# Kernel optimization log

Hardware: AMD Instinct MI355X
Metric: run time of the kernel (lower is better)

Reference implementation:

```python
import jax, jax.numpy as jnp
import numpy as np

N_CELL = 50000
N_GENE = 50000
E = 800000
D = 256
EPS = 1e-5


def setup_inputs() -> dict:
    key = jax.random.key(0)
    ks = jax.random.split(key, 12)
    inp = {
        "x_cell": jax.random.normal(ks[0], (N_CELL, D), jnp.float32),
        "x_gene": jax.random.normal(ks[1], (N_GENE, D), jnp.float32),
        "W_cg": jax.random.normal(ks[2], (D, D), jnp.float32) * (1.0 / np.sqrt(D)),
        "W_gc": jax.random.normal(ks[3], (D, D), jnp.float32) * (1.0 / np.sqrt(D)),
        "W_gg": jax.random.normal(ks[4], (D, D), jnp.float32) * (1.0 / np.sqrt(D)),
        "gamma_cell": jnp.ones((D,), jnp.float32),
        "beta_cell": jnp.zeros((D,), jnp.float32),
        "gamma_gene": jnp.ones((D,), jnp.float32),
        "beta_gene": jnp.zeros((D,), jnp.float32),
        "b_cell": jnp.zeros((D,), jnp.float32),
        "b_gene": jnp.zeros((D,), jnp.float32),
        "src_cg": jax.random.randint(ks[5], (E,), 0, N_CELL, jnp.int64 if jax.config.jax_enable_x64 else jnp.int32),
        "dst_cg": jax.random.randint(ks[6], (E,), 0, N_GENE, jnp.int64 if jax.config.jax_enable_x64 else jnp.int32),
        "src_gc": jax.random.randint(ks[7], (E,), 0, N_GENE, jnp.int64 if jax.config.jax_enable_x64 else jnp.int32),
        "dst_gc": jax.random.randint(ks[8], (E,), 0, N_CELL, jnp.int64 if jax.config.jax_enable_x64 else jnp.int32),
        "src_gg": jax.random.randint(ks[9], (E,), 0, N_GENE, jnp.int64 if jax.config.jax_enable_x64 else jnp.int32),
        "dst_gg": jax.random.randint(ks[10], (E,), 0, N_GENE, jnp.int64 if jax.config.jax_enable_x64 else jnp.int32),
    }
    return inp


def _graph_conv(x_src, src, dst, n_src, n_dst, W):
    """DGL GraphConv with norm='both': D_dst^{-1/2} A D_src^{-1/2} X W."""
    ones = jnp.ones(src.shape[0], x_src.dtype)
    deg_out = jnp.clip(jax.ops.segment_sum(ones, src, num_segments=n_src), 1.0)
    deg_in = jnp.clip(jax.ops.segment_sum(ones, dst, num_segments=n_dst), 1.0)
    h = x_src * jax.lax.rsqrt(deg_out)[:, None]          # [n_src, D]
    agg = jax.ops.segment_sum(h[src], dst, num_segments=n_dst)  # gather+scatter
    agg = agg * jax.lax.rsqrt(deg_in)[:, None]           # [n_dst, D]
    return agg @ W


def _post(h, gamma, beta, b):
    # LayerNorm (affine) -> + h_bias -> relu -> dropout(p=0, eval = identity)
    mu = jnp.mean(h, axis=-1, keepdims=True)
    var = jnp.mean((h - mu) ** 2, axis=-1, keepdims=True)
    h = (h - mu) * jax.lax.rsqrt(var + EPS) * gamma + beta
    return jax.nn.relu(h + b)


def reference(x_cell, x_gene, W_cg, W_gc, W_gg, gamma_cell, beta_cell,
              gamma_gene, beta_gene, b_cell, b_gene,
              src_cg, dst_cg, src_gc, dst_gc, src_gg, dst_gg):
    # HeteroGraphConv with aggregate='sum' across relations per dst ntype
    h_gene = (_graph_conv(x_cell, src_cg, dst_cg, N_CELL, N_GENE, W_cg)
              + _graph_conv(x_gene, src_gg, dst_gg, N_GENE, N_GENE, W_gg))
    h_cell = _graph_conv(x_gene, src_gc, dst_gc, N_GENE, N_CELL, W_gc)
    out_cell = _post(h_cell, gamma_cell, beta_cell, b_cell)
    out_gene = _post(h_gene, gamma_gene, beta_gene, b_gene)
    return jnp.stack([out_cell, out_gene])  # [2, 50000, 256]
```

## Files before the change

### kernel.cpp

```cpp
#include <hip/hip_runtime.h>
#include <hip/hip_bf16.h>
#include <stdint.h>

#define DDIM 256
#define NSHARD 8
#define T1 4096
#define NCPAD 128
#define CCAP 9216

typedef short s8v __attribute__((ext_vector_type(8)));
typedef float f4v __attribute__((ext_vector_type(4)));

__device__ __forceinline__ float bf2f(unsigned u) { return __uint_as_float(u << 16); }
__device__ __forceinline__ unsigned short f2bf(float f) {
    __hip_bfloat16 h = __float2bfloat16(f);
    return *reinterpret_cast<unsigned short*>(&h);
}
__device__ __forceinline__ unsigned pack2(float a, float b) {
    return (unsigned)f2bf(a) | ((unsigned)f2bf(b) << 16);
}

__global__ void transpose3_k(const float* __restrict__ W0, const float* __restrict__ W1,
                             const float* __restrict__ W2, __hip_bfloat16* __restrict__ T0,
                             __hip_bfloat16* __restrict__ T1v, __hip_bfloat16* __restrict__ T2) {
    const float* W = (blockIdx.y == 0) ? W0 : (blockIdx.y == 1) ? W1 : W2;
    __hip_bfloat16* T = (blockIdx.y == 0) ? T0 : (blockIdx.y == 1) ? T1v : T2;
    T[blockIdx.x * DDIM + threadIdx.x] = __float2bfloat16(W[threadIdx.x * DDIM + blockIdx.x]);
}

__global__ __launch_bounds__(256) void bin1_k(
    const int* __restrict__ s0, const int* __restrict__ d0,
    const int* __restrict__ s1, const int* __restrict__ d1,
    const int* __restrict__ s2, const int* __restrict__ d2,
    int* __restrict__ cs_shard,
    int* __restrict__ gcur,
    unsigned* __restrict__ recs,
    int N, int E) {
    __shared__ unsigned stage[T1];
    __shared__ int hcnt[NCPAD], hoff[NCPAD], lbase[NCPAD], lcur[NCPAD];
    const int t = threadIdx.x;
    const int rel = blockIdx.y;
    const int* s = (rel == 0) ? s0 : (rel == 1) ? s1 : s2;
    const int* d = (rel == 0) ? d0 : (rel == 1) ? d1 : d2;
    const int e0 = blockIdx.x * T1;
    const int n = min(T1, E - e0);
    int* csb = cs_shard + ((size_t)(blockIdx.x & (NSHARD - 1)) * 3 + rel) * N;

    if (t < NCPAD) { hcnt[t] = 0; lcur[t] = 0; }
    __syncthreads();

    int ssr[T1 / 256], ddr[T1 / 256];
    #pragma unroll
    for (int k = 0; k < T1 / 256; ++k) {
        const int li = k * 256 + t;
        const bool v = li < n;
        ssr[k] = v ? s[e0 + li] : -1;
        ddr[k] = v ? d[e0 + li] : -1;
        if (v) {
            atomicAdd(&hcnt[ddr[k] >> 9], 1);
            atomicAdd(&csb[ssr[k]], 1);
        }
    }
    __syncthreads();

    if (t < 64) {
        const int a0 = hcnt[2 * t], a1 = hcnt[2 * t + 1];
        const int sum = a0 + a1;
        int incl = sum;
        #pragma unroll
        for (int off = 1; off < 64; off <<= 1) {
            const int u = __shfl_up(incl, off);
            if (t >= off) incl += u;
        }
        const int excl = incl - sum;
        hoff[2 * t] = excl;
        hoff[2 * t + 1] = excl + a0;
    }
    __syncthreads();
    if (t < NCPAD) lbase[t] = atomicAdd(&gcur[rel * NCPAD + t], hcnt[t]);
    __syncthreads();

    #pragma unroll
    for (int k = 0; k < T1 / 256; ++k) {
        if (ddr[k] >= 0) {
            const int b = ddr[k] >> 9;
            const int p = atomicAdd(&lcur[b], 1);
            stage[hoff[b] + p] = (unsigned)ssr[k] | ((unsigned)(ddr[k] & 511) << 16)
                                 | ((unsigned)b << 25);
        }
    }
    __syncthreads();

    for (int i = t; i < n; i += 256) {
        const unsigned r = stage[i];
        const int b = (int)(r >> 25);
        const int pos = lbase[b] + (i - hoff[b]);
        if (pos < CCAP)
            recs[((size_t)rel * NCPAD + b) * CCAP + pos] = r & 0x1FFFFFFu;
    }
}

__device__ __forceinline__ int deg_sum(const int* __restrict__ cs_shard, int rel, int r, int N) {
    int v = 0;
    #pragma unroll
    for (int s = 0; s < NSHARD; ++s) v += cs_shard[((size_t)s * 3 + rel) * N + r];
    return v;
}


__device__ void sort_body(int sb, unsigned char* smem,
                          const unsigned* __restrict__ recs32,
                          unsigned short* __restrict__ recs16,
                          const int* __restrict__ gcur,
                          int* __restrict__ row_beg, int* __restrict__ row_cnt,
                          int N, int ncb) {
    unsigned short* stage = (unsigned short*)smem;
    int* rc   = (int*)(smem + 18432);
    int* ro   = (int*)(smem + 20480);
    int* rcur = (int*)(smem + 22528);
    const int t = threadIdx.x;
    const int rel = sb / ncb, bin = sb % ncb;
    const size_t base = ((size_t)rel * NCPAD + bin) * CCAP;
    const int n = min(gcur[rel * NCPAD + bin], CCAP);

    for (int i = t; i < 512; i += 256) rc[i] = 0;
    __syncthreads();
    for (int i = t; i < n; i += 256)
        atomicAdd(&rc[(recs32[base + i] >> 16) & 511], 1);
    __syncthreads();
    if (t < 64) {
        int v[8], p[8], sum = 0;
        #pragma unroll
        for (int j = 0; j < 8; ++j) { v[j] = rc[t * 8 + j]; p[j] = sum; sum += v[j]; }
        int incl = sum;
        #pragma unroll
        for (int off = 1; off < 64; off <<= 1) {
            const int u = __shfl_up(incl, off);
            if (t >= off) incl += u;
        }
        const int excl = incl - sum;
        #pragma unroll
        for (int j = 0; j < 8; ++j) { ro[t * 8 + j] = excl + p[j]; rcur[t * 8 + j] = excl + p[j]; }
    }
    __syncthreads();
    for (int i = t; i < 512; i += 256) {
        const int grow = bin * 512 + i;
        if (grow < N) {
            row_cnt[(size_t)rel * N + grow] = rc[i];
            row_beg[(size_t)rel * N + grow] = (int)(base + ro[i]);
        }
    }
    for (int i = t; i < n; i += 256) {
        const unsigned r = recs32[base + i];
        const int pos = atomicAdd(&rcur[(r >> 16) & 511], 1);
        stage[pos] = (unsigned short)(r & 0xffffu);
    }
    __syncthreads();
    for (int i = t; i < n; i += 256)
        recs16[base + i] = stage[i];
}

__device__ void gemm2_body(int gb, unsigned char* smem, const float* __restrict__ X,
                           const __hip_bfloat16* __restrict__ Wt0,
                           const __hip_bfloat16* __restrict__ Wt1,
                           const int* __restrict__ cs_shard, int rel0, int rel1,
                           __hip_bfloat16* __restrict__ Y0, __hip_bfloat16* __restrict__ Y1,
                           int M, int N) {
    typedef __hip_bfloat16 (*lds_t)[2][16][DDIM];
    lds_t wlds = (lds_t)smem;
    const int t = threadIdx.x;
    const int lane = t & 63, wid = t >> 6;
    const int c = lane & 15, kb = lane >> 4;
    const int rA = gb * 128 + wid * 32 + c;
    const int rB = rA + 16;
    const bool vA = rA < M, vB = rB < M;
    const int rAc = vA ? rA : (M - 1), rBc = vB ? rB : (M - 1);

    s8v xfA[8], xfB[8];
    const float* xA = X + (size_t)rAc * DDIM;
    const float* xB = X + (size_t)rBc * DDIM;
    #pragma unroll
    for (int ks = 0; ks < 8; ++ks) {
        const int k0 = ks * 32 + kb * 8;
        const f4v a0 = *reinterpret_cast<const f4v*>(xA + k0);
        const f4v a1 = *reinterpret_cast<const f4v*>(xA + k0 + 4);
        const f4v b0 = *reinterpret_cast<const f4v*>(xB + k0);
        const f4v b1 = *reinterpret_cast<const f4v*>(xB + k0 + 4);
        union { s8v v; unsigned short u[8]; } fa, fb;
        #pragma unroll
        for (int j = 0; j < 4; ++j) {
            fa.u[j] = f2bf(a0[j]); fa.u[4 + j] = f2bf(a1[j]);
            fb.u[j] = f2bf(b0[j]); fb.u[4 + j] = f2bf(b1[j]);
        }
        xfA[ks] = fa.v; xfB[ks] = fb.v;
    }

    const int dA0 = deg_sum(cs_shard, rel0, rAc, N), dB0 = deg_sum(cs_shard, rel0, rBc, N);
    const int dA1 = deg_sum(cs_shard, rel1, rAc, N), dB1 = deg_sum(cs_shard, rel1, rBc, N);
    const float s0A = rsqrtf((float)(dA0 < 1 ? 1 : dA0));
    const float s0B = rsqrtf((float)(dB0 < 1 ? 1 : dB0));
    const float s1A = rsqrtf((float)(dA1 < 1 ? 1 : dA1));
    const float s1B = rsqrtf((float)(dB1 < 1 ? 1 : dB1));

    {
        #pragma unroll
        for (int j = 0; j < 4; ++j) {
            const int q = t + j * 256;
            const int rel = q >> 9, rt = (q >> 5) & 15, ch = q & 31;
            const __hip_bfloat16* Wsrc = rel ? Wt1 : Wt0;
            const uint4 v = *reinterpret_cast<const uint4*>(Wsrc + (size_t)rt * DDIM + ch * 8);
            *reinterpret_cast<uint4*>(&(*wlds)[0 * 2 + rel][rt][(ch ^ (rt & 7)) * 8]) = v;
        }
    }

    #pragma unroll 2
    for (int nt = 0; nt < 16; ++nt) {
        __syncthreads();
        uint4 sv[4];
        if (nt + 1 < 16) {
            #pragma unroll
            for (int j = 0; j < 4; ++j) {
                const int q = t + j * 256;
                const int rel = q >> 9, rt = (q >> 5) & 15, ch = q & 31;
                const __hip_bfloat16* Wsrc = rel ? Wt1 : Wt0;
                sv[j] = *reinterpret_cast<const uint4*>(
                    Wsrc + (size_t)((nt + 1) * 16 + rt) * DDIM + ch * 8);
            }
        }

        const int buf = nt & 1;
        f4v a00 = (f4v){0.f,0.f,0.f,0.f}, a01 = a00, a10 = a00, a11 = a00;
        #pragma unroll
        for (int ks = 0; ks < 8; ++ks) {
            const int chs = ((kb + 4 * ks) ^ (c & 7)) * 8;
            const s8v wf0 = *reinterpret_cast<const s8v*>(&(*wlds)[buf * 2 + 0][c][chs]);
            const s8v wf1 = *reinterpret_cast<const s8v*>(&(*wlds)[buf * 2 + 1][c][chs]);
            a00 = __builtin_amdgcn_mfma_f32_16x16x32_bf16(wf0, xfA[ks], a00, 0, 0, 0);
            a10 = __builtin_amdgcn_mfma_f32_16x16x32_bf16(wf0, xfB[ks], a10, 0, 0, 0);
            a01 = __builtin_amdgcn_mfma_f32_16x16x32_bf16(wf1, xfA[ks], a01, 0, 0, 0);
            a11 = __builtin_amdgcn_mfma_f32_16x16x32_bf16(wf1, xfB[ks], a11, 0, 0, 0);
        }
        const int col = nt * 16 + kb * 4;
        if (vA) {
            uint2 o0, o1;
            o0.x = pack2(a00[0] * s0A, a00[1] * s0A); o0.y = pack2(a00[2] * s0A, a00[3] * s0A);
            o1.x = pack2(a01[0] * s1A, a01[1] * s1A); o1.y = pack2(a01[2] * s1A, a01[3] * s1A);
            *reinterpret_cast<uint2*>(Y0 + (size_t)rA * DDIM + col) = o0;
            *reinterpret_cast<uint2*>(Y1 + (size_t)rA * DDIM + col) = o1;
        }
        if (vB) {
            uint2 o0, o1;
            o0.x = pack2(a10[0] * s0B, a10[1] * s0B); o0.y = pack2(a10[2] * s0B, a10[3] * s0B);
            o1.x = pack2(a11[0] * s1B, a11[1] * s1B); o1.y = pack2(a11[2] * s1B, a11[3] * s1B);
            *reinterpret_cast<uint2*>(Y0 + (size_t)rB * DDIM + col) = o0;
            *reinterpret_cast<uint2*>(Y1 + (size_t)rB * DDIM + col) = o1;
        }

        if (nt + 1 < 16) {
            #pragma unroll
            for (int j = 0; j < 4; ++j) {
                const int q = t + j * 256;
                const int rel = q >> 9, rt = (q >> 5) & 15, ch = q & 31;
                *reinterpret_cast<uint4*>(&(*wlds)[(buf ^ 1) * 2 + rel][rt][(ch ^ (rt & 7)) * 8]) = sv[j];
            }
        }
    }
}

__device__ void gemm1_body(int gb, unsigned char* smem, const float* __restrict__ X,
                           const __hip_bfloat16* __restrict__ Wt0,
                           const int* __restrict__ cs_shard, int rel0,
                           __hip_bfloat16* __restrict__ Y0, int M, int N) {
    typedef __hip_bfloat16 (*lds_t)[16][DDIM];
    lds_t wlds = (lds_t)smem;
    const int t = threadIdx.x;
    const int lane = t & 63, wid = t >> 6;
    const int c = lane & 15, kb = lane >> 4;
    const int rA = gb * 128 + wid * 32 + c;
    const int rB = rA + 16;
    const bool vA = rA < M, vB = rB < M;
    const int rAc = vA ? rA : (M - 1), rBc = vB ? rB : (M - 1);

    s8v xfA[8], xfB[8];
    const float* xA = X + (size_t)rAc * DDIM;
    const float* xB = X + (size_t)rBc * DDIM;
    #pragma unroll
    for (int ks = 0; ks < 8; ++ks) {
        const int k0 = ks * 32 + kb * 8;
        const f4v a0 = *reinterpret_cast<const f4v*>(xA + k0);
        const f4v a1 = *reinterpret_cast<const f4v*>(xA + k0 + 4);
        const f4v b0 = *reinterpret_cast<const f4v*>(xB + k0);
        const f4v b1 = *reinterpret_cast<const f4v*>(xB + k0 + 4);
        union { s8v v; unsigned short u[8]; } fa, fb;
        #pragma unroll
        for (int j = 0; j < 4; ++j) {
            fa.u[j] = f2bf(a0[j]); fa.u[4 + j] = f2bf(a1[j]);
            fb.u[j] = f2bf(b0[j]); fb.u[4 + j] = f2bf(b1[j]);
        }
        xfA[ks] = fa.v; xfB[ks] = fb.v;
    }
    const int dA0 = deg_sum(cs_shard, rel0, rAc, N), dB0 = deg_sum(cs_shard, rel0, rBc, N);
    const float s0A = rsqrtf((float)(dA0 < 1 ? 1 : dA0));
    const float s0B = rsqrtf((float)(dB0 < 1 ? 1 : dB0));

    {
        #pragma unroll
        for (int j = 0; j < 2; ++j) {
            const int q = t + j * 256;
            const int rt = (q >> 5) & 15, ch = q & 31;
            const uint4 v = *reinterpret_cast<const uint4*>(Wt0 + (size_t)rt * DDIM + ch * 8);
            *reinterpret_cast<uint4*>(&(*wlds)[0 * 16 + rt][(ch ^ (rt & 7)) * 8]) = v;
        }
    }

    #pragma unroll 2
    for (int nt = 0; nt < 16; ++nt) {
        __syncthreads();
        uint4 sv[2];
        if (nt + 1 < 16) {
            #pragma unroll
            for (int j = 0; j < 2; ++j) {
                const int q = t + j * 256;
                const int rt = (q >> 5) & 15, ch = q & 31;
                sv[j] = *reinterpret_cast<const uint4*>(
                    Wt0 + (size_t)((nt + 1) * 16 + rt) * DDIM + ch * 8);
            }
        }

        const int buf = nt & 1;
        f4v a00 = (f4v){0.f,0.f,0.f,0.f}, a10 = a00;
        #pragma unroll
        for (int ks = 0; ks < 8; ++ks) {
            const int chs = ((kb + 4 * ks) ^ (c & 7)) * 8;
            const s8v wf0 = *reinterpret_cast<const s8v*>(&(*wlds)[buf * 16 + c][chs]);
            a00 = __builtin_amdgcn_mfma_f32_16x16x32_bf16(wf0, xfA[ks], a00, 0, 0, 0);
            a10 = __builtin_amdgcn_mfma_f32_16x16x32_bf16(wf0, xfB[ks], a10, 0, 0, 0);
        }
        const int col = nt * 16 + kb * 4;
        if (vA) {
            uint2 o;
            o.x = pack2(a00[0] * s0A, a00[1] * s0A); o.y = pack2(a00[2] * s0A, a00[3] * s0A);
            *reinterpret_cast<uint2*>(Y0 + (size_t)rA * DDIM + col) = o;
        }
        if (vB) {
            uint2 o;
            o.x = pack2(a10[0] * s0B, a10[1] * s0B); o.y = pack2(a10[2] * s0B, a10[3] * s0B);
            *reinterpret_cast<uint2*>(Y0 + (size_t)rB * DDIM + col) = o;
        }

        if (nt + 1 < 16) {
            #pragma unroll
            for (int j = 0; j < 2; ++j) {
                const int q = t + j * 256;
                const int rt = (q >> 5) & 15, ch = q & 31;
                *reinterpret_cast<uint4*>(&(*wlds)[(buf ^ 1) * 16 + rt][(ch ^ (rt & 7)) * 8]) = sv[j];
            }
        }
    }
}

__global__ __launch_bounds__(256, 2) void mid_k(
    const unsigned* __restrict__ recs32, unsigned short* __restrict__ recs16,
    const int* __restrict__ gcur,
    int* __restrict__ row_beg, int* __restrict__ row_cnt,
    const float* __restrict__ x_gene, const float* __restrict__ x_cell,
    const __hip_bfloat16* __restrict__ Wt_gc, const __hip_bfloat16* __restrict__ Wt_gg,
    const __hip_bfloat16* __restrict__ Wt_cg,
    const int* __restrict__ cs_shard,
    __hip_bfloat16* __restrict__ Y_gc, __hip_bfloat16* __restrict__ Y_gg,
    __hip_bfloat16* __restrict__ Y_cg,
    int N, int ncb, int gemmBlocks) {
    __shared__ uint4 smem4[2048];
    unsigned char* smem = (unsigned char*)smem4;
    const int bid = blockIdx.x;
    if (bid < gemmBlocks) {
        gemm2_body(bid, smem, x_gene, Wt_gc, Wt_gg, cs_shard, 0, 2, Y_gc, Y_gg, N, N);
    } else if (bid < 2 * gemmBlocks) {
        gemm1_body(bid - gemmBlocks, smem, x_cell, Wt_cg, cs_shard, 1, Y_cg, N, N);
    } else {
        sort_body(bid - 2 * gemmBlocks, smem, recs32, recs16, gcur,
                  row_beg, row_cnt, N, ncb);
    }
}

__device__ __forceinline__ void addv(f4v& a, uint2 v) {
    a[0] += bf2f(v.x & 0xffffu);
    a[1] += bf2f(v.x >> 16);
    a[2] += bf2f(v.y & 0xffffu);
    a[3] += bf2f(v.y >> 16);
}

__device__ __forceinline__ f4v segsum(const unsigned short* __restrict__ recs, int beg, int n,
                                      const __hip_bfloat16* __restrict__ Y, int lane) {
    f4v a = (f4v){0.f, 0.f, 0.f, 0.f};
    for (int j0 = 0; j0 < n; j0 += 64) {
        const int chunk = min(64, n - j0);
        unsigned rv = 0;
        if (lane < chunk) rv = recs[beg + j0 + lane];
        int t = 0;
        for (; t + 8 <= chunk; t += 8) {
            uint2 v[8];
            #pragma unroll
            for (int i = 0; i < 8; ++i) {
                const int s = (int)__shfl(rv, t + i);
                v[i] = reinterpret_cast<const uint2*>(Y + (size_t)s * DDIM)[lane];
            }
            #pragma unroll
            for (int i = 0; i < 8; ++i) addv(a, v[i]);
        }
        if (t + 4 <= chunk) {
            uint2 v[4];
            #pragma unroll
            for (int i = 0; i < 4; ++i) {
                const int s = (int)__shfl(rv, t + i);
                v[i] = reinterpret_cast<const uint2*>(Y + (size_t)s * DDIM)[lane];
            }
            #pragma unroll
            for (int i = 0; i < 4; ++i) addv(a, v[i]);
            t += 4;
        }
        for (; t < chunk; ++t) {
            const int s = (int)__shfl(rv, t);
            addv(a, reinterpret_cast<const uint2*>(Y + (size_t)s * DDIM)[lane]);
        }
    }
    return a;
}

__global__ __launch_bounds__(256, 4) void gather_ln_k(
    const unsigned short* __restrict__ recs,
    const int* __restrict__ beg0, const int* __restrict__ cnt0,
    const __hip_bfloat16* __restrict__ Y0,
    const int* __restrict__ beg1, const int* __restrict__ cnt1,
    const __hip_bfloat16* __restrict__ Y1,
    const float* __restrict__ gamma, const float* __restrict__ beta,
    const float* __restrict__ bias, float* __restrict__ out, int n_dst) {
    const int lane = threadIdx.x & 63, wid = threadIdx.x >> 6;
    const int row = blockIdx.x * 4 + wid;
    if (row >= n_dst) return;

    const int n0 = cnt0[row];
    f4v a = segsum(recs, beg0[row], n0, Y0, lane);
    a *= rsqrtf((float)(n0 < 1 ? 1 : n0));
    if (beg1 != nullptr) {
        const int n1 = cnt1[row];
        f4v a1 = segsum(recs, beg1[row], n1, Y1, lane);
        a += a1 * rsqrtf((float)(n1 < 1 ? 1 : n1));
    }

    float s1 = a[0] + a[1] + a[2] + a[3];
    float s2 = a[0]*a[0] + a[1]*a[1] + a[2]*a[2] + a[3]*a[3];
    #pragma unroll
    for (int off = 1; off < 64; off <<= 1) {
        s1 += __shfl_xor(s1, off);
        s2 += __shfl_xor(s2, off);
    }
    const float mu = s1 * (1.f / 256.f);
    float var = s2 * (1.f / 256.f) - mu * mu;
    var = fmaxf(var, 0.f);
    const float rs = rsqrtf(var + 1e-5f);

    const f4v g  = reinterpret_cast<const f4v*>(gamma)[lane];
    const f4v be = reinterpret_cast<const f4v*>(beta)[lane];
    const f4v bb = reinterpret_cast<const f4v*>(bias)[lane];
    f4v o;
    #pragma unroll
    for (int j = 0; j < 4; ++j) {
        float v = (a[j] - mu) * rs * g[j] + be[j] + bb[j];
        o[j] = fmaxf(v, 0.f);
    }
    reinterpret_cast<f4v*>(out + (size_t)row * DDIM)[lane] = o;
}

extern "C" void kernel_launch(void* const* d_in, const int* in_sizes, int n_in,
                              void* d_out, int out_size, void* d_ws, size_t ws_size,
                              hipStream_t stream) {
    const float* x_cell     = (const float*)d_in[0];
    const float* x_gene     = (const float*)d_in[1];
    const float* W_cg       = (const float*)d_in[2];
    const float* W_gc       = (const float*)d_in[3];
    const float* W_gg       = (const float*)d_in[4];
    const float* gamma_cell = (const float*)d_in[5];
    const float* beta_cell  = (const float*)d_in[6];
    const float* gamma_gene = (const float*)d_in[7];
    const float* beta_gene  = (const float*)d_in[8];
    const float* b_cell     = (const float*)d_in[9];
    const float* b_gene     = (const float*)d_in[10];
    const int* src_cg = (const int*)d_in[11];
    const int* dst_cg = (const int*)d_in[12];
    const int* src_gc = (const int*)d_in[13];
    const int* dst_gc = (const int*)d_in[14];
    const int* src_gg = (const int*)d_in[15];
    const int* dst_gg = (const int*)d_in[16];

    const int N = in_sizes[0] / DDIM;
    const int E = in_sizes[11];
    const int ncb = (N + 511) >> 9;

    char* wsb = (char*)d_ws;
    size_t off = 0;
    __hip_bfloat16* Y_gc = (__hip_bfloat16*)(wsb + off); off += (size_t)N * DDIM * 2;
    unsigned* recs32 = (unsigned*)(wsb + off);           off += (size_t)3 * NCPAD * CCAP * 4;
    unsigned short* recs16 = (unsigned short*)(wsb + off); off += (size_t)3 * NCPAD * CCAP * 2;
    int* row_beg = (int*)(wsb + off);                    off += (size_t)3 * N * 4;
    int* row_cnt = (int*)(wsb + off);                    off += (size_t)3 * N * 4;
    const size_t zeroOff = off;
    int* cs_shard = (int*)(wsb + off);                   off += (size_t)NSHARD * 3 * N * 4;
    int* gcur     = (int*)(wsb + off);                   off += (size_t)3 * NCPAD * 4;
    const size_t zeroBytes = off - zeroOff;
    __hip_bfloat16* Wt_gc = (__hip_bfloat16*)(wsb + off); off += (size_t)DDIM * DDIM * 2;
    __hip_bfloat16* Wt_cg = (__hip_bfloat16*)(wsb + off); off += (size_t)DDIM * DDIM * 2;
    __hip_bfloat16* Wt_gg = (__hip_bfloat16*)(wsb + off);

    int* beg_gc = row_beg, *beg_cg = row_beg + N, *beg_gg = row_beg + 2 * N;
    int* cnt_gc = row_cnt, *cnt_cg = row_cnt + N, *cnt_gg = row_cnt + 2 * N;

    float* out_cell = (float*)d_out;
    float* out_gene = out_cell + (size_t)N * DDIM;
    __hip_bfloat16* Y_cg = (__hip_bfloat16*)d_out;
    __hip_bfloat16* Y_gg = Y_cg + (size_t)N * DDIM;

    const int binBlocks  = (E + T1 - 1) / T1;
    const int gemmBlocks = (N + 127) / 128;
    const int gatherBlocks = (N + 3) / 4;

    transpose3_k<<<dim3(DDIM, 3), DDIM, 0, stream>>>(W_gc, W_cg, W_gg, Wt_gc, Wt_cg, Wt_gg);
    hipMemsetAsync(wsb + zeroOff, 0, zeroBytes, stream);

    bin1_k<<<dim3(binBlocks, 3), 256, 0, stream>>>(src_gc, dst_gc, src_cg, dst_cg,
                                                   src_gg, dst_gg, cs_shard, gcur, recs32, N, E);

    mid_k<<<2 * gemmBlocks + 3 * ncb, 256, 0, stream>>>(
        recs32, recs16, gcur, row_beg, row_cnt, x_gene, x_cell,
        Wt_gc, Wt_gg, Wt_cg, cs_shard, Y_gc, Y_gg, Y_cg, N, ncb, gemmBlocks);

    gather_ln_k<<<gatherBlocks, 256, 0, stream>>>(recs16, beg_cg, cnt_cg, Y_cg,
                                                  beg_gg, cnt_gg, Y_gg,
                                                  gamma_gene, beta_gene, b_gene, out_gene, N);
    gather_ln_k<<<gatherBlocks, 256, 0, stream>>>(recs16, beg_gc, cnt_gc, Y_gc,
                                                  nullptr, nullptr, nullptr,
                                                  gamma_cell, beta_cell, b_cell, out_cell, N);
}
```

Baseline: 372.9 us.

## Sort CSR bins by row and source sub-bucket for gather locality

The per-bin counting sort now keys each record on its destination row plus a 16-way bucket of the source index's upper bits, so edges within a row come out grouped by source range. The scan is widened to 8192 counters with a two-level wave scan, and records are written straight to global memory instead of going through an LDS staging buffer. The goal is better cache locality for the later gather of source rows, paid for with a bigger histogram, more LDS per block (slightly over 32KB, which may hurt occupancy of the merged kernel) and scattered global 16-bit stores.

```diff
diff --git a/kernel.cpp b/kernel.cpp
--- a/kernel.cpp
+++ b/kernel.cpp
@@ -7,6 +7,7 @@
 #define T1 4096
 #define NCPAD 128
 #define CCAP 9216
+#define SBK 16
 
 typedef short s8v __attribute__((ext_vector_type(8)));
 typedef float f4v __attribute__((ext_vector_type(4)));
@@ -114,50 +115,59 @@
                           const int* __restrict__ gcur,
                           int* __restrict__ row_beg, int* __restrict__ row_cnt,
                           int N, int ncb) {
-    unsigned short* stage = (unsigned short*)smem;
-    int* rc   = (int*)(smem + 18432);
-    int* ro   = (int*)(smem + 20480);
-    int* rcur = (int*)(smem + 22528);
-    const int t = threadIdx.x;
+    int* rc   = (int*)smem;
+    int* wsum = (int*)(smem + 32768);
+    const int t = threadIdx.x, lane = t & 63, wid = t >> 6;
     const int rel = sb / ncb, bin = sb % ncb;
     const size_t base = ((size_t)rel * NCPAD + bin) * CCAP;
     const int n = min(gcur[rel * NCPAD + bin], CCAP);
 
-    for (int i = t; i < 512; i += 256) rc[i] = 0;
-    __syncthreads();
-    for (int i = t; i < n; i += 256)
-        atomicAdd(&rc[(recs32[base + i] >> 16) & 511], 1);
-    __syncthreads();
-    if (t < 64) {
-        int v[8], p[8], sum = 0;
-        #pragma unroll
-        for (int j = 0; j < 8; ++j) { v[j] = rc[t * 8 + j]; p[j] = sum; sum += v[j]; }
-        int incl = sum;
-        #pragma unroll
-        for (int off = 1; off < 64; off <<= 1) {
-            const int u = __shfl_up(incl, off);
-            if (t >= off) incl += u;
-        }
-        const int excl = incl - sum;
-        #pragma unroll
-        for (int j = 0; j < 8; ++j) { ro[t * 8 + j] = excl + p[j]; rcur[t * 8 + j] = excl + p[j]; }
-    }
-    __syncthreads();
-    for (int i = t; i < 512; i += 256) {
-        const int grow = bin * 512 + i;
-        if (grow < N) {
-            row_cnt[(size_t)rel * N + grow] = rc[i];
-            row_beg[(size_t)rel * N + grow] = (int)(base + ro[i]);
-        }
-    }
+    for (int i = t; i < 512 * SBK; i += 256) rc[i] = 0;
+    __syncthreads();
     for (int i = t; i < n; i += 256) {
         const unsigned r = recs32[base + i];
-        const int pos = atomicAdd(&rcur[(r >> 16) & 511], 1);
-        stage[pos] = (unsigned short)(r & 0xffffu);
-    }
-    __syncthreads();
-    for (int i = t; i < n; i += 256)
-        recs16[base + i] = stage[i];
+        atomicAdd(&rc[((r >> 16) & 511) * SBK + ((r & 0xffffu) >> 12)], 1);
+    }
+    __syncthreads();
+    int vals[32];
+    int lsum = 0;
+    #pragma unroll
+    for (int j = 0; j < 32; ++j) { vals[j] = rc[t * 32 + j]; lsum += vals[j]; }
+    int incl = lsum;
+    #pragma unroll
+    for (int off = 1; off < 64; off <<= 1) {
+        const int u = __shfl_up(incl, off);
+        if (lane >= off) incl += u;
+    }
+    if (lane == 63) wsum[wid] = incl;
+    __syncthreads();
+    int woff = 0;
+    #pragma unroll
+    for (int w = 0; w < 4; ++w) if (w < wid) woff += wsum[w];
+    const int excl = woff + incl - lsum;
+    int run = excl;
+    #pragma unroll
+    for (int j = 0; j < 32; ++j) { const int v = vals[j]; rc[t * 32 + j] = run; run += v; }
+    {
+        int c0 = 0, c1 = 0;
+        #pragma unroll
+        for (int j = 0; j < 16; ++j) { c0 += vals[j]; c1 += vals[16 + j]; }
+        const int g0 = bin * 512 + 2 * t;
+        if (g0 < N) {
+            row_cnt[(size_t)rel * N + g0] = c0;
+            row_beg[(size_t)rel * N + g0] = (int)base + excl;
+        }
+        if (g0 + 1 < N) {
+            row_cnt[(size_t)rel * N + g0 + 1] = c1;
+            row_beg[(size_t)rel * N + g0 + 1] = (int)base + excl + c0;
+        }
+    }
+    __syncthreads();
+    for (int i = t; i < n; i += 256) {
+        const unsigned r = recs32[base + i];
+        const int pos = atomicAdd(&rc[((r >> 16) & 511) * SBK + ((r & 0xffffu) >> 12)], 1);
+        recs16[base + pos] = (unsigned short)(r & 0xffffu);
+    }
 }
 
 __device__ void gemm2_body(int gb, unsigned char* smem, const float* __restrict__ X,
@@ -370,7 +380,7 @@
     __hip_bfloat16* __restrict__ Y_gc, __hip_bfloat16* __restrict__ Y_gg,
     __hip_bfloat16* __restrict__ Y_cg,
     int N, int ncb, int gemmBlocks) {
-    __shared__ uint4 smem4[2048];
+    __shared__ uint4 smem4[2051];
     unsigned char* smem = (unsigned char*)smem4;
     const int bid = blockIdx.x;
     if (bid < gemmBlocks) {
```

New measurement: 378.8 us. Within noise of the previous version (+1.6%).
